# Optimization experiments

Hardware: AMD Instinct MI355X
Metric: run time of the kernel (lower is better)

Reference implementation:

```python
import jax, jax.numpy as jnp
import numpy as np

FP8_MAX = 448.0  # finfo(float8_e4m3fn).max
EPS = 1e-12
BLK = 128        # weight_block_size = (128, 128); activation group_size = 128


def setup_inputs() -> dict:
    key = jax.random.key(0)
    k1, k2, k3, k4 = jax.random.split(key, 4)
    B, S, H, O = 4, 4096, 2048, 2048
    x = jax.random.normal(k1, (B, S, H), dtype=jnp.float32)
    # fp8 weight: generate, round to e4m3fn grid, store as f32 (values exactly fp8-representable)
    w_raw = jax.random.normal(k2, (O, H), dtype=jnp.float32) * 0.02
    weight = w_raw.astype(jnp.float8_e4m3fn).astype(jnp.float32)
    # per-(128x128)-block weight scales
    weight_scale = jax.random.uniform(k3, (O // BLK, H // BLK), dtype=jnp.float32,
                                      minval=0.001, maxval=0.01)
    bias = jax.random.normal(k4, (O,), dtype=jnp.float32) * 0.01
    return {"x": x, "weight": weight, "weight_scale": weight_scale, "bias": bias}


def reference(x, weight, weight_scale, bias):
    B, S, H = x.shape
    O = weight.shape[0]
    J = H // BLK  # number of activation groups / weight column-blocks
    # per-token-group fp8 quantization (group_size = BLK)
    xg = x.reshape(-1, J, BLK)                                      # [M, J, BLK]
    max_abs = jnp.clip(jnp.max(jnp.abs(xg), axis=-1, keepdims=True), EPS)
    scales = FP8_MAX / max_abs                                      # [M, J, 1]
    xq = jnp.clip(xg * scales, -FP8_MAX, FP8_MAX)
    xq = xq.astype(jnp.float8_e4m3fn).astype(jnp.float32)           # fp8 round-trip
    inv_scale = 1.0 / scales                                        # stored input_scale
    # block-scaled matmul == dequantize both operands then single GEMM
    x_dq = (xq * inv_scale).reshape(-1, H)                          # [M, H]
    w_scale_full = jnp.repeat(jnp.repeat(weight_scale, BLK, axis=0), BLK, axis=1)  # [O, H]
    w_dq = weight * w_scale_full                                    # [O, H]
    y = x_dq @ w_dq.T + bias                                        # [M, O]
    return y.reshape(B, S, O)
```

## Files before the change

### kernel.cpp

```cpp
#include <hip/hip_runtime.h>
#include <cstdint>

#define FP8MAX 448.0f

typedef float f32x4 __attribute__((ext_vector_type(4)));
typedef int   i32x4 __attribute__((ext_vector_type(4)));
typedef int   i32x8 __attribute__((ext_vector_type(8)));

union frag8 { i32x8 v8; i32x4 v4[2]; };

__device__ __forceinline__ void gload_lds16(const void* g, void* l) {
  __builtin_amdgcn_global_load_lds(
      (const __attribute__((address_space(1))) unsigned int*)g,
      (__attribute__((address_space(3))) unsigned int*)l,
      16, 0, 0);
}

__global__ __launch_bounds__(256) void quant_x(const float* __restrict__ x,
                                               uint8_t* __restrict__ xq,
                                               float* __restrict__ sa) {
  const int m = blockIdx.x;
  const int t = threadIdx.x;
  const float* xr = x + (size_t)m * 2048;
  float4 v0 = ((const float4*)xr)[t * 2];
  float4 v1 = ((const float4*)xr)[t * 2 + 1];
  float amax = fmaxf(fmaxf(fmaxf(fabsf(v0.x), fabsf(v0.y)), fmaxf(fabsf(v0.z), fabsf(v0.w))),
                     fmaxf(fmaxf(fabsf(v1.x), fabsf(v1.y)), fmaxf(fabsf(v1.z), fabsf(v1.w))));
  #pragma unroll
  for (int off = 1; off < 16; off <<= 1)
    amax = fmaxf(amax, __shfl_xor(amax, off));
  amax = fmaxf(amax, 1e-12f);
  float s   = FP8MAX / amax;
  float inv = 1.0f / s;
  if ((t & 15) == 0) sa[(size_t)m * 16 + (t >> 4)] = inv;
  float q[8] = {v0.x * s, v0.y * s, v0.z * s, v0.w * s,
                v1.x * s, v1.y * s, v1.z * s, v1.w * s};
  #pragma unroll
  for (int i = 0; i < 8; ++i) q[i] = fminf(fmaxf(q[i], -FP8MAX), FP8MAX);
  union { unsigned long long u; unsigned int w[2]; } pk;
  pk.w[0] = __builtin_amdgcn_cvt_pk_fp8_f32(q[0], q[1], 0, false);
  pk.w[0] = __builtin_amdgcn_cvt_pk_fp8_f32(q[2], q[3], pk.w[0], true);
  pk.w[1] = __builtin_amdgcn_cvt_pk_fp8_f32(q[4], q[5], 0, false);
  pk.w[1] = __builtin_amdgcn_cvt_pk_fp8_f32(q[6], q[7], pk.w[1], true);
  ((unsigned long long*)(xq + (size_t)m * 2048))[t] = pk.u;
}

__global__ __launch_bounds__(256) void conv_w(const float* __restrict__ w,
                                              uint8_t* __restrict__ w8, int n8) {
  int i = blockIdx.x * 256 + threadIdx.x;
  if (i >= n8) return;
  float4 v0 = ((const float4*)w)[i * 2];
  float4 v1 = ((const float4*)w)[i * 2 + 1];
  union { unsigned long long u; unsigned int x[2]; } pk;
  pk.x[0] = __builtin_amdgcn_cvt_pk_fp8_f32(v0.x, v0.y, 0, false);
  pk.x[0] = __builtin_amdgcn_cvt_pk_fp8_f32(v0.z, v0.w, pk.x[0], true);
  pk.x[1] = __builtin_amdgcn_cvt_pk_fp8_f32(v1.x, v1.y, 0, false);
  pk.x[1] = __builtin_amdgcn_cvt_pk_fp8_f32(v1.z, v1.w, pk.x[1], true);
  ((unsigned long long*)w8)[i] = pk.u;
}

__global__ __launch_bounds__(512, 4) void gemm_fp8(
    const uint8_t* __restrict__ A, const uint8_t* __restrict__ Bw,
    const float* __restrict__ sa, const float* __restrict__ sb,
    const float* __restrict__ bias, float* __restrict__ out,
    int M, int N, int K) {
  const int J = K >> 7;
  const int nbn = N >> 7;
  int bid = blockIdx.x;
  int nwg = gridDim.x;
  if ((nwg & 7) == 0) {
    int cpx = nwg >> 3;
    bid = (bid & 7) * cpx + (bid >> 3);
  }
  const int bn = bid % nbn;
  const int bm = bid / nbn;
  const int t = threadIdx.x;
  const int lane = t & 63;
  const int w = t >> 6;
  const int wr = w >> 1;
  const int wc = w & 1;
  const int r16 = lane & 15;
  const int kg = lane >> 4;

  __shared__ __align__(16) uint8_t lA[2][128 * 128];
  __shared__ __align__(16) uint8_t lB[2][128 * 128];
  __shared__ __align__(16) float sal[16 * 128];

  const uint8_t* gA = A + (size_t)bm * 128 * K;
  const uint8_t* gB = Bw + (size_t)bn * 128 * K;

  for (int i = t; i < 128 * 16; i += 512) {
    int row = i >> 4, j = i & 15;
    sal[j * 128 + row] = sa[((size_t)bm * 128 + row) * 16 + j];
  }

  const int rl = t >> 3;
  const int sg = t & 7;

  #define STAGE(buf_, kt_) do {                                              \
    _Pragma("unroll")                                                        \
    for (int it_ = 0; it_ < 2; ++it_) {                                      \
      int r_ = it_ * 64 + rl;                                                \
      int so_ = ((sg ^ (r_ & 7)) << 4);                                      \
      gload_lds16(gA + (size_t)r_ * K + ((kt_) << 7) + so_,                  \
                  &lA[buf_][r_ * 128 + sg * 16]);                            \
      gload_lds16(gB + (size_t)r_ * K + ((kt_) << 7) + so_,                  \
                  &lB[buf_][r_ * 128 + sg * 16]);                            \
    } } while (0)

  __syncthreads();

  STAGE(0, 0);
  STAGE(1, 1);

  f32x4 tot[2][4] = {};
  const f32x4 fz = {0.f, 0.f, 0.f, 0.f};
  frag8 av[2], bv[4];
  f32x4 scq[2];

  const int KT = K >> 7;
  for (int kt = 0; kt < KT; ++kt) {
    const int cur = kt & 1;
    asm volatile("s_waitcnt vmcnt(4)" ::: "memory");
    __builtin_amdgcn_s_barrier();
    asm volatile("" ::: "memory");
    #pragma unroll
    for (int a = 0; a < 2; ++a) {
      int row = wr * 32 + a * 16 + r16;
      const uint8_t* bp = &lA[cur][row * 128];
      int sw = (row & 7) << 4;
      av[a].v4[0] = *(const i32x4*)(bp + ((kg * 32) ^ sw));
      av[a].v4[1] = *(const i32x4*)(bp + ((kg * 32 + 16) ^ sw));
    }
    #pragma unroll
    for (int b = 0; b < 4; ++b) {
      int row = wc * 64 + b * 16 + r16;
      const uint8_t* bp = &lB[cur][row * 128];
      int sw = (row & 7) << 4;
      bv[b].v4[0] = *(const i32x4*)(bp + ((kg * 32) ^ sw));
      bv[b].v4[1] = *(const i32x4*)(bp + ((kg * 32 + 16) ^ sw));
    }
    const float sbj = sb[bn * J + kt];
    #pragma unroll
    for (int a = 0; a < 2; ++a)
      scq[a] = (*(const f32x4*)&sal[kt * 128 + wr * 32 + a * 16 + kg * 4]) * sbj;
    __builtin_amdgcn_s_setprio(1);
    #pragma unroll
    for (int a = 0; a < 2; ++a) {
      #pragma unroll
      for (int b = 0; b < 4; ++b) {
        f32x4 p = __builtin_amdgcn_mfma_scale_f32_16x16x128_f8f6f4(
            av[a].v8, bv[b].v8, fz, 0, 0, 0, 0x7f7f7f7f, 0, 0x7f7f7f7f);
        tot[a][b] += p * scq[a];
      }
    }
    __builtin_amdgcn_s_setprio(0);
    __builtin_amdgcn_s_barrier();
    asm volatile("" ::: "memory");
    const int kt2 = (kt + 2 < KT) ? kt + 2 : kt + 2 - KT;
    STAGE(cur, kt2);
  }
  asm volatile("s_waitcnt vmcnt(0)" ::: "memory");

  float bb[4];
  #pragma unroll
  for (int b = 0; b < 4; ++b) bb[b] = bias[bn * 128 + wc * 64 + b * 16 + r16];
  #pragma unroll
  for (int a = 0; a < 2; ++a) {
    int row0 = bm * 128 + wr * 32 + a * 16 + kg * 4;
    #pragma unroll
    for (int r = 0; r < 4; ++r) {
      float* orow = out + (size_t)(row0 + r) * N + bn * 128 + wc * 64;
      #pragma unroll
      for (int b = 0; b < 4; ++b)
        orow[b * 16 + r16] = tot[a][b][r] + bb[b];
    }
  }
}

extern "C" void kernel_launch(void* const* d_in, const int* in_sizes, int n_in,
                              void* d_out, int out_size, void* d_ws, size_t ws_size,
                              hipStream_t stream) {
  const float* x    = (const float*)d_in[0];
  const float* wt   = (const float*)d_in[1];
  const float* wsc  = (const float*)d_in[2];
  const float* bias = (const float*)d_in[3];
  float* out = (float*)d_out;

  const int O = in_sizes[3];
  const int H = in_sizes[1] / O;
  const int M = in_sizes[0] / H;

  uint8_t* xq = (uint8_t*)d_ws;
  uint8_t* w8 = xq + (size_t)M * H;
  float*   sa = (float*)(w8 + (size_t)O * H);

  quant_x<<<M, 256, 0, stream>>>(x, xq, sa);
  int n8 = O * H / 8;
  conv_w<<<(n8 + 255) / 256, 256, 0, stream>>>(wt, w8, n8);
  int grid = (M / 128) * (O / 128);
  gemm_fp8<<<grid, 512, 0, stream>>>(xq, w8, sa, wsc, bias, out, M, O, H);
}
```

Before: 142.1 us.

## Load A fragments directly to registers and halve workgroup to 4 waves

The GEMM kernel drops the LDS staging buffer for the activation tile. Each wave now loads its 64x128 A fragments straight from global memory into registers, double-buffered across two unrolled k-steps. The workgroup shrinks from 512 to 256 threads, so each wave computes a 64x64 output tile with 16 MFMAs per k-step, and only B stays staged in LDS. This removes LDS traffic and capacity for A and raises per-wave register reuse, at the cost of more VGPR pressure and unswizzled direct global loads for A.

New measurement: 542.7 us. 3.82x slower.

```diff
diff --git a/kernel.cpp b/kernel.cpp
--- a/kernel.cpp
+++ b/kernel.cpp
@@ -59,7 +59,7 @@
   ((unsigned long long*)w8)[i] = pk.u;
 }
 
-__global__ __launch_bounds__(512, 4) void gemm_fp8(
+__global__ __launch_bounds__(256, 3) void gemm_fp8(
     const uint8_t* __restrict__ A, const uint8_t* __restrict__ Bw,
     const float* __restrict__ sa, const float* __restrict__ sb,
     const float* __restrict__ bias, float* __restrict__ out,
@@ -82,98 +82,101 @@
   const int r16 = lane & 15;
   const int kg = lane >> 4;
 
-  __shared__ __align__(16) uint8_t lA[2][128 * 128];
   __shared__ __align__(16) uint8_t lB[2][128 * 128];
   __shared__ __align__(16) float sal[16 * 128];
 
   const uint8_t* gA = A + (size_t)bm * 128 * K;
   const uint8_t* gB = Bw + (size_t)bn * 128 * K;
 
-  for (int i = t; i < 128 * 16; i += 512) {
+  for (int i = t; i < 128 * 16; i += 256) {
     int row = i >> 4, j = i & 15;
     sal[j * 128 + row] = sa[((size_t)bm * 128 + row) * 16 + j];
   }
 
-  const int rl = t >> 3;
   const int sg = t & 7;
 
-  #define STAGE(buf_, kt_) do {                                              \
-    _Pragma("unroll")                                                        \
-    for (int it_ = 0; it_ < 2; ++it_) {                                      \
-      int r_ = it_ * 64 + rl;                                                \
-      int so_ = ((sg ^ (r_ & 7)) << 4);                                      \
-      gload_lds16(gA + (size_t)r_ * K + ((kt_) << 7) + so_,                  \
-                  &lA[buf_][r_ * 128 + sg * 16]);                            \
-      gload_lds16(gB + (size_t)r_ * K + ((kt_) << 7) + so_,                  \
+  #define STAGEB(buf_, kt_) do {                                             \
+    _Pragma("unroll")                                                        \
+    for (int it_ = 0; it_ < 4; ++it_) {                                      \
+      int r_ = it_ * 32 + (t >> 3);                                          \
+      gload_lds16(gB + (size_t)r_ * K + ((kt_) << 7) + ((sg ^ (r_ & 7)) << 4),\
                   &lB[buf_][r_ * 128 + sg * 16]);                            \
     } } while (0)
 
+  #define LOADA(dst_, kt_) do {                                              \
+    _Pragma("unroll")                                                        \
+    for (int a_ = 0; a_ < 4; ++a_) {                                         \
+      const uint8_t* p_ = gA + (size_t)(wr * 64 + a_ * 16 + r16) * K +       \
+                          ((kt_) << 7) + kg * 32;                            \
+      dst_[a_].v4[0] = *(const i32x4*)p_;                                    \
+      dst_[a_].v4[1] = *(const i32x4*)(p_ + 16);                             \
+    } } while (0)
+
   __syncthreads();
 
-  STAGE(0, 0);
-  STAGE(1, 1);
-
-  f32x4 tot[2][4] = {};
+  frag8 avA[4], avB[4], bv[4];
+  f32x4 tot[4][4] = {};
+  f32x4 scq[4];
   const f32x4 fz = {0.f, 0.f, 0.f, 0.f};
-  frag8 av[2], bv[4];
-  f32x4 scq[2];
-
   const int KT = K >> 7;
-  for (int kt = 0; kt < KT; ++kt) {
-    const int cur = kt & 1;
-    asm volatile("s_waitcnt vmcnt(4)" ::: "memory");
-    __builtin_amdgcn_s_barrier();
-    asm volatile("" ::: "memory");
-    #pragma unroll
-    for (int a = 0; a < 2; ++a) {
-      int row = wr * 32 + a * 16 + r16;
-      const uint8_t* bp = &lA[cur][row * 128];
-      int sw = (row & 7) << 4;
-      av[a].v4[0] = *(const i32x4*)(bp + ((kg * 32) ^ sw));
-      av[a].v4[1] = *(const i32x4*)(bp + ((kg * 32 + 16) ^ sw));
-    }
-    #pragma unroll
-    for (int b = 0; b < 4; ++b) {
-      int row = wc * 64 + b * 16 + r16;
-      const uint8_t* bp = &lB[cur][row * 128];
-      int sw = (row & 7) << 4;
-      bv[b].v4[0] = *(const i32x4*)(bp + ((kg * 32) ^ sw));
-      bv[b].v4[1] = *(const i32x4*)(bp + ((kg * 32 + 16) ^ sw));
-    }
-    const float sbj = sb[bn * J + kt];
-    #pragma unroll
-    for (int a = 0; a < 2; ++a)
-      scq[a] = (*(const f32x4*)&sal[kt * 128 + wr * 32 + a * 16 + kg * 4]) * sbj;
-    __builtin_amdgcn_s_setprio(1);
-    #pragma unroll
-    for (int a = 0; a < 2; ++a) {
-      #pragma unroll
-      for (int b = 0; b < 4; ++b) {
-        f32x4 p = __builtin_amdgcn_mfma_scale_f32_16x16x128_f8f6f4(
-            av[a].v8, bv[b].v8, fz, 0, 0, 0, 0x7f7f7f7f, 0, 0x7f7f7f7f);
-        tot[a][b] += p * scq[a];
-      }
-    }
-    __builtin_amdgcn_s_setprio(0);
-    __builtin_amdgcn_s_barrier();
-    asm volatile("" ::: "memory");
-    const int kt2 = (kt + 2 < KT) ? kt + 2 : kt + 2 - KT;
-    STAGE(cur, kt2);
+
+  STAGEB(0, 0);
+  LOADA(avA, 0);
+  STAGEB(1, 1);
+
+  #define BODY(kt_, avC_, avN_) do {                                         \
+    const int b_ = (kt_) & 1;                                                \
+    asm volatile("s_waitcnt vmcnt(4)" ::: "memory");                         \
+    __builtin_amdgcn_s_barrier();                                            \
+    asm volatile("" ::: "memory");                                           \
+    _Pragma("unroll")                                                        \
+    for (int j_ = 0; j_ < 4; ++j_) {                                         \
+      int row_ = wc * 64 + j_ * 16 + r16;                                    \
+      const uint8_t* bp_ = &lB[b_][row_ * 128];                              \
+      int sw_ = (row_ & 7) << 4;                                             \
+      bv[j_].v4[0] = *(const i32x4*)(bp_ + ((kg * 32) ^ sw_));               \
+      bv[j_].v4[1] = *(const i32x4*)(bp_ + ((kg * 32 + 16) ^ sw_));          \
+    }                                                                        \
+    const float sbj_ = sb[bn * J + (kt_)];                                   \
+    _Pragma("unroll")                                                        \
+    for (int a_ = 0; a_ < 4; ++a_)                                           \
+      scq[a_] = (*(const f32x4*)&sal[(kt_) * 128 + wr * 64 + a_ * 16 +       \
+                                     kg * 4]) * sbj_;                        \
+    { const int kn_ = ((kt_) + 1 < KT) ? (kt_) + 1 : 0;                      \
+      LOADA(avN_, kn_); }                                                    \
+    __builtin_amdgcn_s_setprio(1);                                           \
+    _Pragma("unroll")                                                        \
+    for (int a_ = 0; a_ < 4; ++a_) { _Pragma("unroll")                       \
+      for (int j_ = 0; j_ < 4; ++j_) {                                       \
+        f32x4 p_ = __builtin_amdgcn_mfma_scale_f32_16x16x128_f8f6f4(         \
+            avC_[a_].v8, bv[j_].v8, fz, 0, 0, 0, 0x7f7f7f7f, 0, 0x7f7f7f7f); \
+        tot[a_][j_] += p_ * scq[a_];                                         \
+      } }                                                                    \
+    __builtin_amdgcn_s_setprio(0);                                           \
+    __builtin_amdgcn_s_barrier();                                            \
+    asm volatile("" ::: "memory");                                           \
+    { const int k2_ = ((kt_) + 2 < KT) ? (kt_) + 2 : (kt_) + 2 - KT;         \
+      STAGEB(b_, k2_); }                                                     \
+  } while (0)
+
+  for (int kt = 0; kt < KT; kt += 2) {
+    BODY(kt, avA, avB);
+    BODY(kt + 1, avB, avA);
   }
   asm volatile("s_waitcnt vmcnt(0)" ::: "memory");
 
   float bb[4];
   #pragma unroll
-  for (int b = 0; b < 4; ++b) bb[b] = bias[bn * 128 + wc * 64 + b * 16 + r16];
-  #pragma unroll
-  for (int a = 0; a < 2; ++a) {
-    int row0 = bm * 128 + wr * 32 + a * 16 + kg * 4;
+  for (int j = 0; j < 4; ++j) bb[j] = bias[bn * 128 + wc * 64 + j * 16 + r16];
+  #pragma unroll
+  for (int a = 0; a < 4; ++a) {
+    int row0 = bm * 128 + wr * 64 + a * 16 + kg * 4;
     #pragma unroll
     for (int r = 0; r < 4; ++r) {
       float* orow = out + (size_t)(row0 + r) * N + bn * 128 + wc * 64;
       #pragma unroll
-      for (int b = 0; b < 4; ++b)
-        orow[b * 16 + r16] = tot[a][b][r] + bb[b];
+      for (int j = 0; j < 4; ++j)
+        orow[j * 16 + r16] = tot[a][j][r] + bb[j];
     }
   }
 }
@@ -199,5 +202,5 @@
   int n8 = O * H / 8;
   conv_w<<<(n8 + 255) / 256, 256, 0, stream>>>(wt, w8, n8);
   int grid = (M / 128) * (O / 128);
-  gemm_fp8<<<grid, 512, 0, stream>>>(xq, w8, sa, wsc, bias, out, M, O, H);
-}
+  gemm_fp8<<<grid, 256, 0, stream>>>(xq, w8, sa, wsc, bias, out, M, O, H);
+}
```

## Use 4 waves per block with 64x64 warp tiles in FP8 GEMM

Applied to the files above, without the earlier changes.

Cuts the GEMM workgroup from 512 to 256 threads, so each of the 4 waves now computes a 64x64 sub-tile (4x4 MFMAs) instead of 32x64. Each wave now issues 4 global-to-LDS loads per operand per stage instead of 2, and the vmcnt wait is adjusted to match. This raises per-wave register reuse of A/B fragments and reduces the LDS reads per MFMA. In exchange it uses more accumulator registers and leaves fewer waves to hide latency.

After: 147.7 us. +3.9%, slower.

```diff
diff --git a/kernel.cpp b/kernel.cpp
--- a/kernel.cpp
+++ b/kernel.cpp
@@ -59,7 +59,7 @@
   ((unsigned long long*)w8)[i] = pk.u;
 }
 
-__global__ __launch_bounds__(512, 4) void gemm_fp8(
+__global__ __launch_bounds__(256, 2) void gemm_fp8(
     const uint8_t* __restrict__ A, const uint8_t* __restrict__ Bw,
     const float* __restrict__ sa, const float* __restrict__ sb,
     const float* __restrict__ bias, float* __restrict__ out,
@@ -77,8 +77,8 @@
   const int t = threadIdx.x;
   const int lane = t & 63;
   const int w = t >> 6;
-  const int wr = w >> 1;
-  const int wc = w & 1;
+  const int wm = (w >> 1) << 6;
+  const int wn = (w & 1) << 6;
   const int r16 = lane & 15;
   const int kg = lane >> 4;
 
@@ -89,18 +89,18 @@
   const uint8_t* gA = A + (size_t)bm * 128 * K;
   const uint8_t* gB = Bw + (size_t)bn * 128 * K;
 
-  for (int i = t; i < 128 * 16; i += 512) {
-    int row = i >> 4, j = i & 15;
+  for (int i = t; i < 128 * 16; i += 256) {
+    int row = i & 127, j = i >> 7;
     sal[j * 128 + row] = sa[((size_t)bm * 128 + row) * 16 + j];
   }
 
-  const int rl = t >> 3;
+  const int srow = t >> 3;
   const int sg = t & 7;
 
   #define STAGE(buf_, kt_) do {                                              \
     _Pragma("unroll")                                                        \
-    for (int it_ = 0; it_ < 2; ++it_) {                                      \
-      int r_ = it_ * 64 + rl;                                                \
+    for (int it_ = 0; it_ < 4; ++it_) {                                      \
+      int r_ = srow + it_ * 32;                                              \
       int so_ = ((sg ^ (r_ & 7)) << 4);                                      \
       gload_lds16(gA + (size_t)r_ * K + ((kt_) << 7) + so_,                  \
                   &lA[buf_][r_ * 128 + sg * 16]);                            \
@@ -113,40 +113,44 @@
   STAGE(0, 0);
   STAGE(1, 1);
 
-  f32x4 tot[2][4] = {};
+  f32x4 tot[4][4] = {};
   const f32x4 fz = {0.f, 0.f, 0.f, 0.f};
-  frag8 av[2], bv[4];
-  f32x4 scq[2];
+  frag8 av[4], bv[4];
+  f32x4 scq[4];
+
+  int rowA[4], rowB[4];
+  #pragma unroll
+  for (int a = 0; a < 4; ++a) rowA[a] = wm + a * 16 + r16;
+  #pragma unroll
+  for (int b = 0; b < 4; ++b) rowB[b] = wn + b * 16 + r16;
 
   const int KT = K >> 7;
   for (int kt = 0; kt < KT; ++kt) {
     const int cur = kt & 1;
-    asm volatile("s_waitcnt vmcnt(4)" ::: "memory");
+    asm volatile("s_waitcnt vmcnt(8)" ::: "memory");
     __builtin_amdgcn_s_barrier();
     asm volatile("" ::: "memory");
     #pragma unroll
-    for (int a = 0; a < 2; ++a) {
-      int row = wr * 32 + a * 16 + r16;
-      const uint8_t* bp = &lA[cur][row * 128];
-      int sw = (row & 7) << 4;
+    for (int a = 0; a < 4; ++a) {
+      const int sw = (rowA[a] & 7) << 4;
+      const uint8_t* bp = &lA[cur][rowA[a] * 128];
       av[a].v4[0] = *(const i32x4*)(bp + ((kg * 32) ^ sw));
       av[a].v4[1] = *(const i32x4*)(bp + ((kg * 32 + 16) ^ sw));
     }
     #pragma unroll
     for (int b = 0; b < 4; ++b) {
-      int row = wc * 64 + b * 16 + r16;
-      const uint8_t* bp = &lB[cur][row * 128];
-      int sw = (row & 7) << 4;
+      const int sw = (rowB[b] & 7) << 4;
+      const uint8_t* bp = &lB[cur][rowB[b] * 128];
       bv[b].v4[0] = *(const i32x4*)(bp + ((kg * 32) ^ sw));
       bv[b].v4[1] = *(const i32x4*)(bp + ((kg * 32 + 16) ^ sw));
     }
     const float sbj = sb[bn * J + kt];
     #pragma unroll
-    for (int a = 0; a < 2; ++a)
-      scq[a] = (*(const f32x4*)&sal[kt * 128 + wr * 32 + a * 16 + kg * 4]) * sbj;
+    for (int a = 0; a < 4; ++a)
+      scq[a] = (*(const f32x4*)&sal[kt * 128 + wm + a * 16 + kg * 4]) * sbj;
     __builtin_amdgcn_s_setprio(1);
     #pragma unroll
-    for (int a = 0; a < 2; ++a) {
+    for (int a = 0; a < 4; ++a) {
       #pragma unroll
       for (int b = 0; b < 4; ++b) {
         f32x4 p = __builtin_amdgcn_mfma_scale_f32_16x16x128_f8f6f4(
@@ -164,16 +168,16 @@
 
   float bb[4];
   #pragma unroll
-  for (int b = 0; b < 4; ++b) bb[b] = bias[bn * 128 + wc * 64 + b * 16 + r16];
-  #pragma unroll
-  for (int a = 0; a < 2; ++a) {
-    int row0 = bm * 128 + wr * 32 + a * 16 + kg * 4;
+  for (int b = 0; b < 4; ++b) bb[b] = bias[bn * 128 + wn + b * 16 + r16];
+  #pragma unroll
+  for (int a = 0; a < 4; ++a) {
+    int row0 = bm * 128 + wm + a * 16 + kg * 4;
     #pragma unroll
     for (int r = 0; r < 4; ++r) {
-      float* orow = out + (size_t)(row0 + r) * N + bn * 128 + wc * 64;
+      float* orow = out + (size_t)(row0 + r) * N + bn * 128;
       #pragma unroll
       for (int b = 0; b < 4; ++b)
-        orow[b * 16 + r16] = tot[a][b][r] + bb[b];
+        orow[wn + b * 16 + r16] = tot[a][b][r] + bb[b];
     }
   }
 }
@@ -199,5 +203,5 @@
   int n8 = O * H / 8;
   conv_w<<<(n8 + 255) / 256, 256, 0, stream>>>(wt, w8, n8);
   int grid = (M / 128) * (O / 128);
-  gemm_fp8<<<grid, 512, 0, stream>>>(xq, w8, sa, wsc, bias, out, M, O, H);
-}
+  gemm_fp8<<<grid, 256, 0, stream>>>(xq, w8, sa, wsc, bias, out, M, O, H);
+}
```
